# Optimization experiments

Measured on AMD Instinct MI355X. Metric: run time of the kernel, lower is better.

## Reference

```python
import jax, jax.numpy as jnp
import numpy as np

EMBED_DIM = 1024
NUM_HEADS = 16
HEAD_DIM = EMBED_DIM // NUM_HEADS  # 64
SCALE = HEAD_DIM ** -0.5


def _rope_table(seq_len, dtype=jnp.float32):
    # inv_freq: [head_dim/2]
    inv_freq = 1.0 / (10000.0 ** (jnp.arange(0, HEAD_DIM, 2, dtype=dtype) / HEAD_DIM))
    t = jnp.arange(seq_len, dtype=dtype)
    freqs = t[:, None] * inv_freq[None, :]  # [S, hd/2]
    return jnp.sin(freqs), jnp.cos(freqs)


def _apply_rope(x, sin, cos):
    # x: [B, H, S, hd]; sin/cos: [S, hd/2]
    sin = sin[None, None]
    cos = cos[None, None]
    x_even = x[..., 0::2]
    x_odd = x[..., 1::2]
    new_even = x_even * cos - x_odd * sin
    new_odd = x_even * sin + x_odd * cos
    # interleave back: [..., hd/2, 2] -> [..., hd]
    return jnp.stack((new_even, new_odd), axis=-1).reshape(x.shape)


def setup_inputs() -> dict:
    key = jax.random.key(0)
    ks = jax.random.split(key, 9)
    B, S, D = 2, 2048, EMBED_DIM
    s = D ** -0.5
    return {
        "query": jax.random.normal(ks[0], (B, S, D), dtype=jnp.float32),
        "Wq": jax.random.normal(ks[1], (2 * D, D), dtype=jnp.float32) * s,
        "bq": jnp.zeros((2 * D,), dtype=jnp.float32),
        "Wk": jax.random.normal(ks[2], (D, D), dtype=jnp.float32) * s,
        "bk": jnp.zeros((D,), dtype=jnp.float32),
        "Wv": jax.random.normal(ks[3], (D, D), dtype=jnp.float32) * s,
        "bv": jnp.zeros((D,), dtype=jnp.float32),
        "Wo": jax.random.normal(ks[4], (D, D), dtype=jnp.float32) * s,
        "bo": jnp.zeros((D,), dtype=jnp.float32),
    }


def reference(query, Wq, bq, Wk, bk, Wv, bv, Wo, bo):
    B, S, D = query.shape
    H, hd = NUM_HEADS, HEAD_DIM

    # QKV projections (elementwise-gate variant: q_proj outputs 2*D)
    q_raw = (query @ Wq.T + bq).reshape(B, S, H, 2 * hd)
    q = q_raw[..., :hd].transpose(0, 2, 1, 3)          # [B,H,S,hd]
    gate = q_raw[..., hd:].transpose(0, 2, 1, 3)        # [B,H,S,hd]
    k = (query @ Wk.T + bk).reshape(B, S, H, hd).transpose(0, 2, 1, 3)
    v = (query @ Wv.T + bv).reshape(B, S, H, hd).transpose(0, 2, 1, 3)

    sin, cos = _rope_table(S)
    q = _apply_rope(q, sin, cos)
    k = _apply_rope(k, sin, cos)

    # scaled dot-product attention (no mask, non-causal, dropout=0)
    scores = jnp.einsum('bhqd,bhkd->bhqk', q, k) * SCALE
    probs = jax.nn.softmax(scores, axis=-1)
    attn = jnp.einsum('bhqk,bhkd->bhqd', probs, v)

    # sigmoid elementwise gate, then output projection
    attn = attn * jax.nn.sigmoid(gate)
    out = attn.transpose(0, 2, 1, 3).reshape(B, S, D)
    return out @ Wo.T + bo
```

## Files before the change

### kernel.cpp

```cpp
#include <hip/hip_runtime.h>
#include <math.h>

#define SEQ 2048
#define DIMD 1024
#define NH 16
#define HDIM 64

typedef _Float16 h8 __attribute__((ext_vector_type(8)));
typedef _Float16 h4 __attribute__((ext_vector_type(4)));
typedef __fp16 fp16x2 __attribute__((ext_vector_type(2)));
typedef float f32x4 __attribute__((ext_vector_type(4)));

typedef const __attribute__((address_space(1))) void* gas_t;
typedef __attribute__((address_space(3))) void* las_t;

__device__ __forceinline__ int SWE(int r, int c) {
  return ((r << 6) + c) ^ ((r & 7) << 3);
}

#define R0 16384
#define R1 (R0 + 1048576)
#define R2 (R1 + 524288)
#define R3 (R2 + 262144)
#define R4 (R3 + 262144)
#define R5 (R4 + 262144)

__global__ void prep_kernel(const float* __restrict__ query,
                            const float* __restrict__ Wq,
                            const float* __restrict__ Wk,
                            const float* __restrict__ Wv,
                            const float* __restrict__ Wo,
                            _Float16* __restrict__ Ah,
                            _Float16* __restrict__ Wqh,
                            _Float16* __restrict__ Wkh,
                            _Float16* __restrict__ Wvh,
                            _Float16* __restrict__ Woh,
                            float* __restrict__ sintab,
                            float* __restrict__ costab) {
  int i = blockIdx.x * 256 + threadIdx.x;
  if (i < R0) {
#pragma unroll
    for (int j = 0; j < 4; ++j) {
      int idx = i * 4 + j;
      int tp = idx >> 5;
      int fi = idx & 31;
      double inv = pow(10000.0, -(double)(2 * fi) / 64.0);
      double a = (double)tp * inv;
      sintab[idx] = (float)sin(a);
      costab[idx] = (float)cos(a);
    }
    return;
  }
  const float* src;
  _Float16* dst;
  int k;
  if (i < R1) {
    k = i - R0; src = query; dst = Ah;
  } else if (i < R2) {
    k = i - R1; src = Wq; dst = Wqh;
  } else if (i < R3) {
    k = i - R2; src = Wk; dst = Wkh;
  } else if (i < R4) {
    k = i - R3; src = Wv; dst = Wvh;
  } else if (i < R5) {
    k = i - R4; src = Wo; dst = Woh;
  } else {
    return;
  }
  float4 v = ((const float4*)src)[k];
  h4 H;
  H[0] = (_Float16)v.x;
  H[1] = (_Float16)v.y;
  H[2] = (_Float16)v.z;
  H[3] = (_Float16)v.w;
  ((h4*)dst)[k] = H;
}

__global__ __launch_bounds__(256) void qkv_kernel(
    const _Float16* __restrict__ Ah, const _Float16* __restrict__ Wqh,
    const _Float16* __restrict__ Wkh, const _Float16* __restrict__ Wvh,
    const float* __restrict__ bq, const float* __restrict__ bk,
    const float* __restrict__ bv, _Float16* __restrict__ qw,
    _Float16* __restrict__ sg, _Float16* __restrict__ kw,
    _Float16* __restrict__ vtw, const float* __restrict__ sintab,
    const float* __restrict__ costab) {
  __shared__ _Float16 Abuf[8192];
  __shared__ _Float16 Bbuf[8192];
  const int t = threadIdx.x;
  const int lane = t & 63;
  const int w = t >> 6;
  const int wm = w & 1, wn = w >> 1;
  const int fr = lane & 15;
  const int g = lane >> 4;
  const int m0 = blockIdx.y * 128;
  const int n0 = blockIdx.x * 128;
  const int region = (n0 < 2048) ? 0 : (n0 < 3072 ? 1 : 2);
  const _Float16* Wb = region == 0   ? Wqh + (size_t)n0 * DIMD
                       : region == 1 ? Wkh + (size_t)(n0 - 2048) * DIMD
                                     : Wvh + (size_t)(n0 - 3072) * DIMD;
  const float* bias = region == 0   ? bq + n0
                      : region == 1 ? bk + (n0 - 2048)
                                    : bv + (n0 - 3072);

  f32x4 acc[4][4];
#pragma unroll
  for (int i = 0; i < 4; ++i)
#pragma unroll
    for (int j = 0; j < 4; ++j) acc[i][j] = (f32x4){0.f, 0.f, 0.f, 0.f};

  const int rsub = t >> 3;
  const int csw = ((t & 7) ^ (rsub & 7)) << 3;
  const _Float16* gA = Ah + (size_t)(m0 + rsub) * DIMD + csw;
  const _Float16* gB = Wb + (size_t)rsub * DIMD + csw;
  const int dbase = (t >> 6) * 512 + 0;

  for (int kt = 0; kt < 16; ++kt) {
#pragma unroll
    for (int i = 0; i < 4; ++i) {
      __builtin_amdgcn_global_load_lds(
          (gas_t)(gA + (size_t)i * 32 * DIMD + kt * 64),
          (las_t)&Abuf[i * 2048 + w * 512], 16, 0, 0);
      __builtin_amdgcn_global_load_lds(
          (gas_t)(gB + (size_t)i * 32 * DIMD + kt * 64),
          (las_t)&Bbuf[i * 2048 + w * 512], 16, 0, 0);
    }
    __syncthreads();
#pragma unroll
    for (int s = 0; s < 2; ++s) {
      h8 av[4], bv[4];
#pragma unroll
      for (int mi = 0; mi < 4; ++mi)
        av[mi] = *(const h8*)&Abuf[SWE(wm * 64 + mi * 16 + fr, 8 * g + 32 * s)];
#pragma unroll
      for (int ni = 0; ni < 4; ++ni)
        bv[ni] = *(const h8*)&Bbuf[SWE(wn * 64 + ni * 16 + fr, 8 * g + 32 * s)];
      __builtin_amdgcn_s_setprio(1);
#pragma unroll
      for (int mi = 0; mi < 4; ++mi)
#pragma unroll
        for (int ni = 0; ni < 4; ++ni)
          acc[mi][ni] = __builtin_amdgcn_mfma_f32_16x16x32_f16(
              av[mi], bv[ni], acc[mi][ni], 0, 0, 0);
      __builtin_amdgcn_s_setprio(0);
    }
    __syncthreads();
  }

#pragma unroll
  for (int mi = 0; mi < 4; ++mi)
#pragma unroll
    for (int ni = 0; ni < 4; ++ni) {
      const int cl = wn * 64 + ni * 16 + fr;
      const float bsv = bias[cl];
      if (region == 2) {
        const int vc = (n0 - 3072) + cl;
        const int h = vc >> 6, d = vc & 63;
        const int row0 = m0 + wm * 64 + mi * 16 + g * 4;
        const int b = row0 >> 11;
        const int s0 = row0 & (SEQ - 1);
        h4 vv;
#pragma unroll
        for (int r = 0; r < 4; ++r) vv[r] = (_Float16)(acc[mi][ni][r] + bsv);
        *(h4*)&vtw[((size_t)(b * NH + h) * HDIM + d) * SEQ + s0] = vv;
        continue;
      }
#pragma unroll
      for (int r = 0; r < 4; ++r) {
        const int row = m0 + wm * 64 + mi * 16 + g * 4 + r;
        float v = acc[mi][ni][r] + bsv;
        const int b = row >> 11;
        const int s = row & (SEQ - 1);
        if (region == 0) {
          const int h = n0 >> 7;
          const int d = cl & 63;
          if (wn == 0) {
            float vp = __shfl_xor(v, 1);
            const int pi = s * 32 + (d >> 1);
            float sn = sintab[pi], cs = costab[pi];
            float rv = (d & 1) ? (vp * sn + v * cs) : (v * cs - vp * sn);
            rv *= 0.125f;
            qw[((size_t)(b * NH + h) * SEQ + s) * HDIM + d] = (_Float16)rv;
          } else {
            float gv = 1.0f / (1.0f + __expf(-v));
            sg[((size_t)(b * SEQ + s)) * DIMD + h * HDIM + d] = (_Float16)gv;
          }
        } else {
          const int kc = (n0 - 2048) + cl;
          const int h = kc >> 6, d = kc & 63;
          float vp = __shfl_xor(v, 1);
          const int pi = s * 32 + (d >> 1);
          float sn = sintab[pi], cs = costab[pi];
          float rv = (d & 1) ? (vp * sn + v * cs) : (v * cs - vp * sn);
          kw[((size_t)(b * NH + h) * SEQ + s) * HDIM + d] = (_Float16)rv;
        }
      }
    }
}

__global__ __launch_bounds__(256) void ogemm_kernel(
    const _Float16* __restrict__ ag, const _Float16* __restrict__ Woh,
    const float* __restrict__ bias, float* __restrict__ out) {
  __shared__ _Float16 Abuf[8192];
  __shared__ _Float16 Bbuf[4096];
  const int t = threadIdx.x;
  const int lane = t & 63;
  const int w = t >> 6;
  const int wm = w & 1, wn = w >> 1;
  const int fr = lane & 15;
  const int g = lane >> 4;
  const int m0 = blockIdx.y * 128, n0 = blockIdx.x * 64;

  f32x4 acc[4][2];
#pragma unroll
  for (int i = 0; i < 4; ++i)
#pragma unroll
    for (int j = 0; j < 2; ++j) acc[i][j] = (f32x4){0.f, 0.f, 0.f, 0.f};

  const int rsub = t >> 3;
  const int csw = ((t & 7) ^ (rsub & 7)) << 3;
  const _Float16* gA = ag + (size_t)(m0 + rsub) * DIMD + csw;
  const _Float16* gB = Woh + (size_t)(n0 + rsub) * DIMD + csw;

  for (int kt = 0; kt < 16; ++kt) {
#pragma unroll
    for (int i = 0; i < 4; ++i)
      __builtin_amdgcn_global_load_lds(
          (gas_t)(gA + (size_t)i * 32 * DIMD + kt * 64),
          (las_t)&Abuf[i * 2048 + w * 512], 16, 0, 0);
#pragma unroll
    for (int i = 0; i < 2; ++i)
      __builtin_amdgcn_global_load_lds(
          (gas_t)(gB + (size_t)i * 32 * DIMD + kt * 64),
          (las_t)&Bbuf[i * 2048 + w * 512], 16, 0, 0);
    __syncthreads();
#pragma unroll
    for (int s = 0; s < 2; ++s) {
      h8 av[4], bv[2];
#pragma unroll
      for (int mi = 0; mi < 4; ++mi)
        av[mi] = *(const h8*)&Abuf[SWE(wm * 64 + mi * 16 + fr, 8 * g + 32 * s)];
#pragma unroll
      for (int ni = 0; ni < 2; ++ni)
        bv[ni] = *(const h8*)&Bbuf[SWE(wn * 32 + ni * 16 + fr, 8 * g + 32 * s)];
      __builtin_amdgcn_s_setprio(1);
#pragma unroll
      for (int mi = 0; mi < 4; ++mi)
#pragma unroll
        for (int ni = 0; ni < 2; ++ni)
          acc[mi][ni] = __builtin_amdgcn_mfma_f32_16x16x32_f16(
              av[mi], bv[ni], acc[mi][ni], 0, 0, 0);
      __builtin_amdgcn_s_setprio(0);
    }
    __syncthreads();
  }

#pragma unroll
  for (int mi = 0; mi < 4; ++mi)
#pragma unroll
    for (int ni = 0; ni < 2; ++ni) {
      const int col = n0 + wn * 32 + ni * 16 + fr;
      const float bsv = bias[col];
#pragma unroll
      for (int r = 0; r < 4; ++r) {
        const int row = m0 + wm * 64 + mi * 16 + g * 4 + r;
        out[(size_t)row * DIMD + col] = acc[mi][ni][r] + bsv;
      }
    }
}

__global__ __launch_bounds__(256) void flash_kernel(
    const _Float16* __restrict__ qh, const _Float16* __restrict__ kh,
    const _Float16* __restrict__ vt, const _Float16* __restrict__ sg,
    _Float16* __restrict__ ag) {
  __shared__ _Float16 K_lds[4096];
  __shared__ _Float16 Vt_lds[4096];
  const int t = threadIdx.x;
  const int lane = t & 63;
  const int w = t >> 6;
  const int fr = lane & 15;
  const int g = lane >> 4;
  const int flat = blockIdx.x;
  const int swz = (flat & 7) * 128 + (flat >> 3);
  const int bh = swz >> 5;
  const int q0 = (swz & 31) * 64;
  const size_t kvbase = (size_t)bh * (SEQ * HDIM);

  h8 qb[2];
  {
    const _Float16* qp = qh + kvbase + (size_t)(q0 + 16 * w + fr) * HDIM + 8 * g;
    qb[0] = *(const h8*)(qp);
    qb[1] = *(const h8*)(qp + 32);
  }

  f32x4 oacc[4];
  float m_i = -1e30f, l_i = 0.f;
#pragma unroll
  for (int df = 0; df < 4; ++df) oacc[df] = (f32x4){0.f, 0.f, 0.f, 0.f};

  const int srow = t >> 2;
  const int scb = (t & 3) * 16;
  const _Float16* kp = kh + kvbase;
  const _Float16* vp = vt + kvbase + (size_t)srow * SEQ;

  h8 k0v = *(const h8*)(kp + (size_t)srow * HDIM + scb);
  h8 k1v = *(const h8*)(kp + (size_t)srow * HDIM + scb + 8);
  h8 v0v = *(const h8*)(vp + scb);
  h8 v1v = *(const h8*)(vp + scb + 8);

  for (int j0 = 0; j0 < SEQ; j0 += 64) {
    __syncthreads();
    *(h8*)&K_lds[SWE(srow, scb)] = k0v;
    *(h8*)&K_lds[SWE(srow, scb + 8)] = k1v;
    *(h8*)&Vt_lds[SWE(srow, scb)] = v0v;
    *(h8*)&Vt_lds[SWE(srow, scb + 8)] = v1v;
    if (j0 + 64 < SEQ) {
      k0v = *(const h8*)(kp + (size_t)(j0 + 64 + srow) * HDIM + scb);
      k1v = *(const h8*)(kp + (size_t)(j0 + 64 + srow) * HDIM + scb + 8);
      v0v = *(const h8*)(vp + j0 + 64 + scb);
      v1v = *(const h8*)(vp + j0 + 64 + scb + 8);
    }
    __syncthreads();

    f32x4 sacc[4];
#pragma unroll
    for (int nf = 0; nf < 4; ++nf) sacc[nf] = (f32x4){0.f, 0.f, 0.f, 0.f};

    __builtin_amdgcn_s_setprio(1);
#pragma unroll
    for (int nf = 0; nf < 4; ++nf) {
      h8 ka0 = *(const h8*)&K_lds[SWE(16 * nf + fr, 8 * g)];
      h8 ka1 = *(const h8*)&K_lds[SWE(16 * nf + fr, 32 + 8 * g)];
      sacc[nf] =
          __builtin_amdgcn_mfma_f32_16x16x32_f16(ka0, qb[0], sacc[nf], 0, 0, 0);
      sacc[nf] =
          __builtin_amdgcn_mfma_f32_16x16x32_f16(ka1, qb[1], sacc[nf], 0, 0, 0);
    }
    __builtin_amdgcn_s_setprio(0);

    float m0 = fmaxf(fmaxf(sacc[0][0], sacc[0][1]), sacc[0][2]);
    float m1 = fmaxf(fmaxf(sacc[0][3], sacc[1][0]), sacc[1][1]);
    float m2 = fmaxf(fmaxf(sacc[1][2], sacc[1][3]), sacc[2][0]);
    float m3 = fmaxf(fmaxf(sacc[2][1], sacc[2][2]), sacc[2][3]);
    float m4 = fmaxf(fmaxf(sacc[3][0], sacc[3][1]), sacc[3][2]);
    float mx =
        fmaxf(fmaxf(fmaxf(fmaxf(m0, m1), m2), fmaxf(m3, m4)), sacc[3][3]);
    mx = fmaxf(mx, __shfl_xor(mx, 16));
    mx = fmaxf(mx, __shfl_xor(mx, 32));
    const int allskip = __all(mx <= m_i + 8.0f);
    const float mn = allskip ? m_i : fmaxf(m_i, mx);
    float p[4][4];
    float rs = 0.f;
#pragma unroll
    for (int nf = 0; nf < 4; ++nf)
#pragma unroll
      for (int r = 0; r < 4; ++r) {
        p[nf][r] = __expf(sacc[nf][r] - mn);
        rs += p[nf][r];
      }
    rs += __shfl_xor(rs, 16);
    rs += __shfl_xor(rs, 32);
    if (allskip) {
      l_i += rs;
    } else {
      float f = __expf(m_i - mn);
      l_i = l_i * f + rs;
      m_i = mn;
      f32x4 fv = (f32x4){f, f, f, f};
#pragma unroll
      for (int df = 0; df < 4; ++df) oacc[df] *= fv;
    }
    h8 pb[2];
#pragma unroll
    for (int m2i = 0; m2i < 2; ++m2i) {
      union {
        h8 v;
        fp16x2 h[4];
      } u;
      u.h[0] = __builtin_amdgcn_cvt_pkrtz(p[2 * m2i][0], p[2 * m2i][1]);
      u.h[1] = __builtin_amdgcn_cvt_pkrtz(p[2 * m2i][2], p[2 * m2i][3]);
      u.h[2] = __builtin_amdgcn_cvt_pkrtz(p[2 * m2i + 1][0], p[2 * m2i + 1][1]);
      u.h[3] = __builtin_amdgcn_cvt_pkrtz(p[2 * m2i + 1][2], p[2 * m2i + 1][3]);
      pb[m2i] = u.v;
    }

    __builtin_amdgcn_s_setprio(1);
#pragma unroll
    for (int df = 0; df < 4; ++df) {
#pragma unroll
      for (int m2i = 0; m2i < 2; ++m2i) {
        h4 vlo = *(const h4*)&Vt_lds[SWE(16 * df + fr, 32 * m2i + 4 * g)];
        h4 vhi = *(const h4*)&Vt_lds[SWE(16 * df + fr, 32 * m2i + 16 + 4 * g)];
        h8 va;
#pragma unroll
        for (int r = 0; r < 4; ++r) {
          va[r] = vlo[r];
          va[4 + r] = vhi[r];
        }
        oacc[df] =
            __builtin_amdgcn_mfma_f32_16x16x32_f16(va, pb[m2i], oacc[df], 0, 0, 0);
      }
    }
    __builtin_amdgcn_s_setprio(0);
  }

  const int b = bh >> 4, h = bh & 15;
  const int qrow = q0 + 16 * w + fr;
  const float inv = 1.0f / l_i;
  const size_t obase = ((size_t)(b * SEQ + qrow)) * DIMD + h * HDIM;
#pragma unroll
  for (int df = 0; df < 4; ++df) {
    const int d0 = 16 * df + 4 * g;
    h4 gt = *(const h4*)&sg[obase + d0];
    h4 ov;
#pragma unroll
    for (int r = 0; r < 4; ++r)
      ov[r] = (_Float16)(oacc[df][r] * inv * (float)gt[r]);
    *(h4*)&ag[obase + d0] = ov;
  }
}

extern "C" void kernel_launch(void* const* d_in, const int* in_sizes, int n_in,
                              void* d_out, int out_size, void* d_ws,
                              size_t ws_size, hipStream_t stream) {
  const float* query = (const float*)d_in[0];
  const float* Wq = (const float*)d_in[1];
  const float* bq = (const float*)d_in[2];
  const float* Wk = (const float*)d_in[3];
  const float* bk = (const float*)d_in[4];
  const float* Wv = (const float*)d_in[5];
  const float* bv = (const float*)d_in[6];
  const float* Wo = (const float*)d_in[7];
  const float* bo = (const float*)d_in[8];
  float* out = (float*)d_out;

  float* fws = (float*)d_ws;
  float* sintab = fws;
  float* costab = fws + 65536;
  _Float16* Ah = (_Float16*)(fws + 131072);
  _Float16* Wqh = Ah + 4194304;
  _Float16* Wkh = Wqh + 2097152;
  _Float16* Wvh = Wkh + 1048576;
  _Float16* Woh = Wvh + 1048576;
  _Float16* qw = Woh + 1048576;
  _Float16* kw = qw + 4194304;
  _Float16* vtw = kw + 4194304;
  _Float16* sg = vtw + 4194304;
  _Float16* ag = Ah;

  prep_kernel<<<9280, 256, 0, stream>>>(query, Wq, Wk, Wv, Wo, Ah, Wqh, Wkh,
                                        Wvh, Woh, sintab, costab);

  qkv_kernel<<<dim3(32, 32), 256, 0, stream>>>(Ah, Wqh, Wkh, Wvh, bq, bk, bv,
                                               qw, sg, kw, vtw, sintab, costab);

  flash_kernel<<<1024, 256, 0, stream>>>(qw, kw, vtw, sg, ag);

  ogemm_kernel<<<dim3(16, 32), 256, 0, stream>>>(ag, Woh, bo, out);
}
```

Measured before the change: 161.6 us.

## Triple-buffer QKV and output GEMMs with async LDS loads and larger tiles

Both GEMM kernels now keep three LDS stages filled by global_load_lds, with explicit vmcnt waits and raw s_barrier, so the next two k-tiles load while the current one is computed. The QKV tile grows to 256x128 and the output GEMM tile to 128x128, halving the grid in each and raising per-block MFMA reuse. The cost is much more LDS per block (about 144KB for QKV), which limits occupancy to one block per CU, and fewer blocks for the output GEMM (256), which may leave CUs underused.

```diff
diff --git a/kernel.cpp b/kernel.cpp
--- a/kernel.cpp
+++ b/kernel.cpp
@@ -84,15 +84,15 @@
     _Float16* __restrict__ sg, _Float16* __restrict__ kw,
     _Float16* __restrict__ vtw, const float* __restrict__ sintab,
     const float* __restrict__ costab) {
-  __shared__ _Float16 Abuf[8192];
-  __shared__ _Float16 Bbuf[8192];
+  __shared__ _Float16 Abuf[3][16384];
+  __shared__ _Float16 Bbuf[3][8192];
   const int t = threadIdx.x;
   const int lane = t & 63;
   const int w = t >> 6;
   const int wm = w & 1, wn = w >> 1;
   const int fr = lane & 15;
   const int g = lane >> 4;
-  const int m0 = blockIdx.y * 128;
+  const int m0 = blockIdx.y * 256;
   const int n0 = blockIdx.x * 128;
   const int region = (n0 < 2048) ? 0 : (n0 < 3072 ? 1 : 2);
   const _Float16* Wb = region == 0   ? Wqh + (size_t)n0 * DIMD
@@ -102,9 +102,9 @@
                       : region == 1 ? bk + (n0 - 2048)
                                     : bv + (n0 - 3072);
 
-  f32x4 acc[4][4];
-#pragma unroll
-  for (int i = 0; i < 4; ++i)
+  f32x4 acc[8][4];
+#pragma unroll
+  for (int i = 0; i < 8; ++i)
 #pragma unroll
     for (int j = 0; j < 4; ++j) acc[i][j] = (f32x4){0.f, 0.f, 0.f, 0.f};
 
@@ -112,42 +112,60 @@
   const int csw = ((t & 7) ^ (rsub & 7)) << 3;
   const _Float16* gA = Ah + (size_t)(m0 + rsub) * DIMD + csw;
   const _Float16* gB = Wb + (size_t)rsub * DIMD + csw;
-  const int dbase = (t >> 6) * 512 + 0;
-
-  for (int kt = 0; kt < 16; ++kt) {
-#pragma unroll
-    for (int i = 0; i < 4; ++i) {
+
+  auto stage = [&](int kt, int bi) {
+#pragma unroll
+    for (int i = 0; i < 8; ++i)
       __builtin_amdgcn_global_load_lds(
           (gas_t)(gA + (size_t)i * 32 * DIMD + kt * 64),
-          (las_t)&Abuf[i * 2048 + w * 512], 16, 0, 0);
+          (las_t)&Abuf[bi][i * 2048 + t * 8], 16, 0, 0);
+#pragma unroll
+    for (int i = 0; i < 4; ++i)
       __builtin_amdgcn_global_load_lds(
           (gas_t)(gB + (size_t)i * 32 * DIMD + kt * 64),
-          (las_t)&Bbuf[i * 2048 + w * 512], 16, 0, 0);
-    }
-    __syncthreads();
-#pragma unroll
-    for (int s = 0; s < 2; ++s) {
-      h8 av[4], bv[4];
-#pragma unroll
-      for (int mi = 0; mi < 4; ++mi)
-        av[mi] = *(const h8*)&Abuf[SWE(wm * 64 + mi * 16 + fr, 8 * g + 32 * s)];
+          (las_t)&Bbuf[bi][i * 2048 + t * 8], 16, 0, 0);
+  };
+
+  stage(0, 0);
+  stage(1, 1);
+  for (int kt = 0; kt < 16; ++kt) {
+    const int cb = kt % 3;
+    if (kt + 2 < 16) {
+      stage(kt + 2, (kt + 2) % 3);
+      asm volatile("s_waitcnt vmcnt(24)" ::: "memory");
+    } else if (kt + 1 < 16) {
+      asm volatile("s_waitcnt vmcnt(12)" ::: "memory");
+    } else {
+      asm volatile("s_waitcnt vmcnt(0)" ::: "memory");
+    }
+    __builtin_amdgcn_sched_barrier(0);
+    __builtin_amdgcn_s_barrier();
+    __builtin_amdgcn_sched_barrier(0);
+#pragma unroll
+    for (int kk = 0; kk < 2; ++kk) {
+      h8 av[8], bv[4];
+#pragma unroll
+      for (int mi = 0; mi < 8; ++mi)
+        av[mi] =
+            *(const h8*)&Abuf[cb][SWE(wm * 128 + mi * 16 + fr, 8 * g + 32 * kk)];
 #pragma unroll
       for (int ni = 0; ni < 4; ++ni)
-        bv[ni] = *(const h8*)&Bbuf[SWE(wn * 64 + ni * 16 + fr, 8 * g + 32 * s)];
+        bv[ni] =
+            *(const h8*)&Bbuf[cb][SWE(wn * 64 + ni * 16 + fr, 8 * g + 32 * kk)];
       __builtin_amdgcn_s_setprio(1);
 #pragma unroll
-      for (int mi = 0; mi < 4; ++mi)
+      for (int mi = 0; mi < 8; ++mi)
 #pragma unroll
         for (int ni = 0; ni < 4; ++ni)
           acc[mi][ni] = __builtin_amdgcn_mfma_f32_16x16x32_f16(
               av[mi], bv[ni], acc[mi][ni], 0, 0, 0);
       __builtin_amdgcn_s_setprio(0);
     }
-    __syncthreads();
-  }
-
-#pragma unroll
-  for (int mi = 0; mi < 4; ++mi)
+    __builtin_amdgcn_s_barrier();
+  }
+
+#pragma unroll
+  for (int mi = 0; mi < 8; ++mi)
 #pragma unroll
     for (int ni = 0; ni < 4; ++ni) {
       const int cl = wn * 64 + ni * 16 + fr;
@@ -155,7 +173,7 @@
       if (region == 2) {
         const int vc = (n0 - 3072) + cl;
         const int h = vc >> 6, d = vc & 63;
-        const int row0 = m0 + wm * 64 + mi * 16 + g * 4;
+        const int row0 = m0 + wm * 128 + mi * 16 + g * 4;
         const int b = row0 >> 11;
         const int s0 = row0 & (SEQ - 1);
         h4 vv;
@@ -166,7 +184,7 @@
       }
 #pragma unroll
       for (int r = 0; r < 4; ++r) {
-        const int row = m0 + wm * 64 + mi * 16 + g * 4 + r;
+        const int row = m0 + wm * 128 + mi * 16 + g * 4 + r;
         float v = acc[mi][ni][r] + bsv;
         const int b = row >> 11;
         const int s = row & (SEQ - 1);
@@ -200,65 +218,82 @@
 __global__ __launch_bounds__(256) void ogemm_kernel(
     const _Float16* __restrict__ ag, const _Float16* __restrict__ Woh,
     const float* __restrict__ bias, float* __restrict__ out) {
-  __shared__ _Float16 Abuf[8192];
-  __shared__ _Float16 Bbuf[4096];
+  __shared__ _Float16 Abuf[3][8192];
+  __shared__ _Float16 Bbuf[3][8192];
   const int t = threadIdx.x;
   const int lane = t & 63;
   const int w = t >> 6;
   const int wm = w & 1, wn = w >> 1;
   const int fr = lane & 15;
   const int g = lane >> 4;
-  const int m0 = blockIdx.y * 128, n0 = blockIdx.x * 64;
-
-  f32x4 acc[4][2];
+  const int m0 = blockIdx.y * 128, n0 = blockIdx.x * 128;
+
+  f32x4 acc[4][4];
 #pragma unroll
   for (int i = 0; i < 4; ++i)
 #pragma unroll
-    for (int j = 0; j < 2; ++j) acc[i][j] = (f32x4){0.f, 0.f, 0.f, 0.f};
+    for (int j = 0; j < 4; ++j) acc[i][j] = (f32x4){0.f, 0.f, 0.f, 0.f};
 
   const int rsub = t >> 3;
   const int csw = ((t & 7) ^ (rsub & 7)) << 3;
   const _Float16* gA = ag + (size_t)(m0 + rsub) * DIMD + csw;
   const _Float16* gB = Woh + (size_t)(n0 + rsub) * DIMD + csw;
 
-  for (int kt = 0; kt < 16; ++kt) {
-#pragma unroll
-    for (int i = 0; i < 4; ++i)
+  auto stage = [&](int kt, int bi) {
+#pragma unroll
+    for (int i = 0; i < 4; ++i) {
       __builtin_amdgcn_global_load_lds(
           (gas_t)(gA + (size_t)i * 32 * DIMD + kt * 64),
-          (las_t)&Abuf[i * 2048 + w * 512], 16, 0, 0);
-#pragma unroll
-    for (int i = 0; i < 2; ++i)
+          (las_t)&Abuf[bi][i * 2048 + t * 8], 16, 0, 0);
       __builtin_amdgcn_global_load_lds(
           (gas_t)(gB + (size_t)i * 32 * DIMD + kt * 64),
-          (las_t)&Bbuf[i * 2048 + w * 512], 16, 0, 0);
-    __syncthreads();
-#pragma unroll
-    for (int s = 0; s < 2; ++s) {
-      h8 av[4], bv[2];
+          (las_t)&Bbuf[bi][i * 2048 + t * 8], 16, 0, 0);
+    }
+  };
+
+  stage(0, 0);
+  stage(1, 1);
+  for (int kt = 0; kt < 16; ++kt) {
+    const int cb = kt % 3;
+    if (kt + 2 < 16) {
+      stage(kt + 2, (kt + 2) % 3);
+      asm volatile("s_waitcnt vmcnt(16)" ::: "memory");
+    } else if (kt + 1 < 16) {
+      asm volatile("s_waitcnt vmcnt(8)" ::: "memory");
+    } else {
+      asm volatile("s_waitcnt vmcnt(0)" ::: "memory");
+    }
+    __builtin_amdgcn_sched_barrier(0);
+    __builtin_amdgcn_s_barrier();
+    __builtin_amdgcn_sched_barrier(0);
+#pragma unroll
+    for (int kk = 0; kk < 2; ++kk) {
+      h8 av[4], bv[4];
 #pragma unroll
       for (int mi = 0; mi < 4; ++mi)
-        av[mi] = *(const h8*)&Abuf[SWE(wm * 64 + mi * 16 + fr, 8 * g + 32 * s)];
-#pragma unroll
-      for (int ni = 0; ni < 2; ++ni)
-        bv[ni] = *(const h8*)&Bbuf[SWE(wn * 32 + ni * 16 + fr, 8 * g + 32 * s)];
+        av[mi] =
+            *(const h8*)&Abuf[cb][SWE(wm * 64 + mi * 16 + fr, 8 * g + 32 * kk)];
+#pragma unroll
+      for (int ni = 0; ni < 4; ++ni)
+        bv[ni] =
+            *(const h8*)&Bbuf[cb][SWE(wn * 64 + ni * 16 + fr, 8 * g + 32 * kk)];
       __builtin_amdgcn_s_setprio(1);
 #pragma unroll
       for (int mi = 0; mi < 4; ++mi)
 #pragma unroll
-        for (int ni = 0; ni < 2; ++ni)
+        for (int ni = 0; ni < 4; ++ni)
           acc[mi][ni] = __builtin_amdgcn_mfma_f32_16x16x32_f16(
               av[mi], bv[ni], acc[mi][ni], 0, 0, 0);
       __builtin_amdgcn_s_setprio(0);
     }
-    __syncthreads();
+    __builtin_amdgcn_s_barrier();
   }
 
 #pragma unroll
   for (int mi = 0; mi < 4; ++mi)
 #pragma unroll
-    for (int ni = 0; ni < 2; ++ni) {
-      const int col = n0 + wn * 32 + ni * 16 + fr;
+    for (int ni = 0; ni < 4; ++ni) {
+      const int col = n0 + wn * 64 + ni * 16 + fr;
       const float bsv = bias[col];
 #pragma unroll
       for (int r = 0; r < 4; ++r) {
@@ -450,10 +485,10 @@
   prep_kernel<<<9280, 256, 0, stream>>>(query, Wq, Wk, Wv, Wo, Ah, Wqh, Wkh,
                                         Wvh, Woh, sintab, costab);
 
-  qkv_kernel<<<dim3(32, 32), 256, 0, stream>>>(Ah, Wqh, Wkh, Wvh, bq, bk, bv,
+  qkv_kernel<<<dim3(32, 16), 256, 0, stream>>>(Ah, Wqh, Wkh, Wvh, bq, bk, bv,
                                                qw, sg, kw, vtw, sintab, costab);
 
   flash_kernel<<<1024, 256, 0, stream>>>(qw, kw, vtw, sg, ag);
 
-  ogemm_kernel<<<dim3(16, 32), 256, 0, stream>>>(ag, Woh, bo, out);
-}
+  ogemm_kernel<<<dim3(8, 32), 256, 0, stream>>>(ag, Woh, bo, out);
+}
```

Result: slower. 199.8 us (+23.7%).
